# Kernel tuning notes

Hardware: AMD Instinct MI355X
Metric: run time of the kernel (lower is better)

## Reference

```python
import jax, jax.numpy as jnp
import numpy as np

N = 50000      # nodes
E = 800000     # edges (before self loops)
IN = 128       # in_ch
HID = 128      # hid (conv1 concat output)
OUT = 128      # out_ch
H = 4          # heads in conv1
NEG_SLOPE = 0.2


def setup_inputs() -> dict:
    key = jax.random.key(0)
    ks = jax.random.split(key, 16)
    s = 0.05
    return {
        "x": jax.random.normal(ks[0], (N, IN), dtype=jnp.float32),
        "edge_index": jax.random.randint(ks[1], (2, E), 0, N, dtype=jnp.int64),
        # conv1 params (heads=4, per-head dim HID//H)
        "W1l": jax.random.normal(ks[2], (IN, HID), dtype=jnp.float32) * s,
        "b1l": jnp.zeros((HID,), jnp.float32),
        "W1r": jax.random.normal(ks[3], (IN, HID), dtype=jnp.float32) * s,
        "b1r": jnp.zeros((HID,), jnp.float32),
        "att1": jax.random.normal(ks[4], (H, HID // H), dtype=jnp.float32) * s,
        "bias1": jnp.zeros((HID,), jnp.float32),
        # conv2 params (heads=1)
        "W2l": jax.random.normal(ks[5], (HID, OUT), dtype=jnp.float32) * s,
        "b2l": jnp.zeros((OUT,), jnp.float32),
        "W2r": jax.random.normal(ks[6], (HID, OUT), dtype=jnp.float32) * s,
        "b2r": jnp.zeros((OUT,), jnp.float32),
        "att2": jax.random.normal(ks[7], (1, OUT), dtype=jnp.float32) * s,
        "bias2": jnp.zeros((OUT,), jnp.float32),
    }


def gatv2_conv(x, src, dst, Wl, bl, Wr, br, att, heads):
    """PyG GATv2Conv (share_weights=False, concat=True).
    message(j->i): e = LeakyReLU(x_l[j] + x_r[i]); logit = <e, att>;
    softmax over edges per destination i; out_i = sum alpha * x_l[j].
    """
    n = x.shape[0]
    c = Wl.shape[1] // heads
    xl = (x @ Wl + bl).reshape(n, heads, c)   # source transform
    xr = (x @ Wr + br).reshape(n, heads, c)   # destination transform
    e = jax.nn.leaky_relu(xl[src] + xr[dst], NEG_SLOPE)      # [E, H, C]
    logits = jnp.einsum("ehc,hc->eh", e, att)                 # [E, H]
    m = jax.lax.stop_gradient(
        jax.ops.segment_max(logits, dst, num_segments=n))     # [N, H]
    p = jnp.exp(logits - m[dst])                              # [E, H]
    denom = jax.ops.segment_sum(p, dst, num_segments=n)       # [N, H]
    alpha = p / denom[dst]                                    # [E, H]
    out = jax.ops.segment_sum(xl[src] * alpha[..., None], dst,
                              num_segments=n)                 # [N, H, C]
    return out.reshape(n, heads * c)


def reference(x, edge_index, W1l, b1l, W1r, b1r, att1, bias1,
              W2l, b2l, W2r, b2r, att2, bias2):
    n = x.shape[0]
    # PyG default add_self_loops=True
    loops = jnp.arange(n, dtype=edge_index.dtype)
    src = jnp.concatenate([edge_index[0], loops])
    dst = jnp.concatenate([edge_index[1], loops])
    h = gatv2_conv(x, src, dst, W1l, b1l, W1r, b1r, att1, H) + bias1
    h = jax.nn.relu(h)
    out = gatv2_conv(h, src, dst, W2l, b2l, W2r, b2r, att2, 1) + bias2
    return out
```

## Files before the change

kernel.cpp:

```cpp
#include <hip/hip_runtime.h>
#include <hip/hip_bf16.h>

#define NODES 50000
#define NEDGE 800000
#define CH 128
#define NEG_SLOPE 0.2f
#define SCAN_CHUNK 2048
#define NBLK ((NODES + SCAN_CHUNK - 1) / SCAN_CHUNK)
#define NINF -1.0e30f
#define LOG2E 1.44269504088896340736f
#define RESCALE_THR 8.0f
#define NSLICE 400
#define SSLICE (NEDGE / NSLICE)
#define ZB ((NODES + 255) / 256)

typedef short short8 __attribute__((ext_vector_type(8)));
typedef float f32x4 __attribute__((ext_vector_type(4)));
typedef float f32x2 __attribute__((ext_vector_type(2)));

__device__ __forceinline__ unsigned fbits(float f) {
    union { float f; unsigned u; } v; v.f = f; return v.u;
}
__device__ __forceinline__ float asf(unsigned u) {
    union { float f; unsigned u; } v; v.u = u; return v.f;
}
__device__ __forceinline__ unsigned short f2bf(float f) {
    unsigned u = fbits(f);
    unsigned r = u + 0x7fff + ((u >> 16) & 1);
    return (unsigned short)(r >> 16);
}
__device__ __forceinline__ float bf2f(unsigned short h) {
    return asf(((unsigned)h) << 16);
}
__device__ __forceinline__ void bf8cvt2(uint4 u, f32x2* f) {
    f[0] = (f32x2){asf(u.x << 16), asf(u.x & 0xFFFF0000u)};
    f[1] = (f32x2){asf(u.y << 16), asf(u.y & 0xFFFF0000u)};
    f[2] = (f32x2){asf(u.z << 16), asf(u.z & 0xFFFF0000u)};
    f[3] = (f32x2){asf(u.w << 16), asf(u.w & 0xFFFF0000u)};
}
__device__ __forceinline__ int dset(int dst) {
    return (int)(((unsigned)dst * 8u) / 50000u);
}

__global__ __launch_bounds__(256) void prep_kernel(const void* idx, int* flag,
                                                   int* cnt,
                                                   const float* __restrict__ W0,
                                                   const float* __restrict__ W1,
                                                   const float* __restrict__ W2,
                                                   const float* __restrict__ W3,
                                                   unsigned short* __restrict__ wbase) {
    int b = (int)blockIdx.x;
    if (b < ZB) {
        int t = b * 256 + (int)threadIdx.x;
        if (t < NODES) cnt[t] = 0;
        if (b == 0 && threadIdx.x < 64) {
            const int* w = (const int*)idx;
            int nz = (w[2 * threadIdx.x + 1] != 0) ? 1 : 0;
            unsigned long long bal = __ballot(nz);
            if (threadIdx.x == 0) *flag = (bal == 0ull) ? 1 : 0;
        }
        return;
    }
    int wb = b - ZB;
    int which = wb >> 6;
    const float* W = (which == 0) ? W0 : (which == 1) ? W1 : (which == 2) ? W2 : W3;
    unsigned short* hiT = wbase + (size_t)which * 32768;
    unsigned short* loT = hiT + 16384;
    int i = (wb & 63) * 256 + (int)threadIdx.x;
    int k = i >> 7, n = i & 127;
    float f = W[i];
    unsigned short h = f2bf(f);
    unsigned short l = f2bf(f - bf2f(h));
    hiT[n * CH + k] = h;
    loT[n * CH + k] = l;
}

__global__ __launch_bounds__(256) void hist_part_kernel(const void* idx,
                                                        const int* flag,
                                                        int* cnt) {
    int set = blockIdx.x & 7;
    int slice = blockIdx.x >> 3;
    int base = slice * SSLICE;
    int endE = base + SSLICE;
    int i64 = *flag;
    const int* w = (const int*)idx;
    for (int e = base + (int)threadIdx.x; e < endE; e += 256) {
        int dst = i64 ? w[2 * (NEDGE + e)] : w[NEDGE + e];
        if (dset(dst) == set) atomicAdd(&cnt[dst], 1);
    }
}

__global__ __launch_bounds__(256) void scan1_kernel(const int* __restrict__ cnt,
                                                    int* __restrict__ bsum) {
    int base = blockIdx.x * SCAN_CHUNK + (int)threadIdx.x * 8;
    int s = 0;
    #pragma unroll
    for (int k = 0; k < 8; ++k) {
        int i = base + k;
        s += (i < NODES) ? cnt[i] : 0;
    }
    #pragma unroll
    for (int m = 1; m < 64; m <<= 1) s += __shfl_xor(s, m);
    __shared__ int ws[4];
    if ((threadIdx.x & 63) == 0) ws[threadIdx.x >> 6] = s;
    __syncthreads();
    if (threadIdx.x == 0) bsum[blockIdx.x] = ws[0] + ws[1] + ws[2] + ws[3];
}

__global__ __launch_bounds__(256) void scan3_kernel(const int* __restrict__ cnt,
                                                    const int* __restrict__ bsum,
                                                    int* __restrict__ offs,
                                                    int* __restrict__ cursor) {
    int tid = (int)threadIdx.x;
    int bpre = 0;
    #pragma unroll
    for (int b = 0; b < NBLK; ++b) bpre += (b < (int)blockIdx.x) ? bsum[b] : 0;

    int base = blockIdx.x * SCAN_CHUNK + tid * 8;
    int v[8];
    int s = 0;
    #pragma unroll
    for (int k = 0; k < 8; ++k) {
        int i = base + k;
        v[k] = (i < NODES) ? cnt[i] : 0;
        s += v[k];
    }
    int lane = tid & 63;
    int incl = s;
    #pragma unroll
    for (int m = 1; m < 64; m <<= 1) {
        int t = __shfl_up(incl, m);
        if (lane >= m) incl += t;
    }
    __shared__ int wtot[4];
    if (lane == 63) wtot[tid >> 6] = incl;
    __syncthreads();
    int w = tid >> 6;
    int wbase = 0;
    #pragma unroll
    for (int k = 0; k < 4; ++k) wbase += (k < w) ? wtot[k] : 0;
    int excl = bpre + wbase + (incl - s);
    #pragma unroll
    for (int k = 0; k < 8; ++k) {
        int i = base + k;
        if (i < NODES) { offs[i] = excl; cursor[i] = excl; }
        excl += v[k];
    }
    if (blockIdx.x == 0 && tid == 0) offs[NODES] = NEDGE;
}

__global__ __launch_bounds__(256) void scatter_part_kernel(const void* idx,
                                                           const int* flag,
                                                           int* cursor,
                                                           int* __restrict__ srcs) {
    int set = blockIdx.x & 7;
    int slice = blockIdx.x >> 3;
    int base = slice * SSLICE;
    int endE = base + SSLICE;
    int i64 = *flag;
    const int* w = (const int*)idx;
    for (int e = base + (int)threadIdx.x; e < endE; e += 256) {
        int dst = i64 ? w[2 * (NEDGE + e)] : w[NEDGE + e];
        if (dset(dst) == set) {
            int src = i64 ? w[2 * e] : w[e];
            int pos = atomicAdd(&cursor[dst], 1);
            srcs[pos] = src;
        }
    }
}

#define GR 64
#define LDP 136

__global__ __launch_bounds__(512) void gemm_dual_mfma(
        const float* __restrict__ X,
        const unsigned short* __restrict__ whTl, const unsigned short* __restrict__ wlTl,
        const unsigned short* __restrict__ whTr, const unsigned short* __restrict__ wlTr,
        const float* __restrict__ bl, const float* __restrict__ br,
        unsigned short* __restrict__ Ylb, float* __restrict__ Yr, int nrows) {
    __shared__ unsigned short xh[GR][LDP];
    __shared__ unsigned short xlo[GR][LDP];

    int r0 = blockIdx.x * GR;
    int tid = (int)threadIdx.x;

    {
        int row = tid >> 3;
        int c0 = (tid & 7) * 16;
        const float* src = X + (size_t)(r0 + row) * CH + c0;
        bool valid = (r0 + row) < nrows;
        #pragma unroll
        for (int j = 0; j < 16; j += 4) {
            float4 v = valid ? *(const float4*)(src + j)
                             : make_float4(0.f, 0.f, 0.f, 0.f);
            unsigned ux = fbits(v.x), uy = fbits(v.y);
            unsigned uz = fbits(v.z), uw = fbits(v.w);
            unsigned hx = ux & 0xFFFF0000u, hy = uy & 0xFFFF0000u;
            unsigned hz = uz & 0xFFFF0000u, hw = uw & 0xFFFF0000u;
            uint2 hp;
            hp.x = (ux >> 16) | hy;
            hp.y = (uz >> 16) | hw;
            float lx = v.x - asf(hx), ly = v.y - asf(hy);
            float lz = v.z - asf(hz), lw = v.w - asf(hw);
            uint2 lp;
            lp.x = (fbits(lx) >> 16) | (fbits(ly) & 0xFFFF0000u);
            lp.y = (fbits(lz) >> 16) | (fbits(lw) & 0xFFFF0000u);
            *(uint2*)&xh[row][c0 + j]  = hp;
            *(uint2*)&xlo[row][c0 + j] = lp;
        }
    }
    __syncthreads();

    int wave = tid >> 6;
    int lane = tid & 63;
    int l15 = lane & 15, q = lane >> 4;

    f32x4 acc[4][2];
    #pragma unroll
    for (int mt = 0; mt < 4; ++mt)
        #pragma unroll
        for (int nt = 0; nt < 2; ++nt) acc[mt][nt] = (f32x4)0.f;

    const unsigned short* bhp[2];
    const unsigned short* blp_[2];
    int ncol[2];
    #pragma unroll
    for (int nt = 0; nt < 2; ++nt) {
        int n = (wave * 2 + nt) * 16 + l15;
        ncol[nt] = n;
        int nn = n & 127;
        bhp[nt]  = ((n < CH) ? whTl : whTr) + (size_t)nn * CH;
        blp_[nt] = ((n < CH) ? wlTl : wlTr) + (size_t)nn * CH;
    }

    for (int kt = 0; kt < 4; ++kt) {
        int kofs = kt * 32 + q * 8;
        short8 ah[4], al[4];
        #pragma unroll
        for (int mt = 0; mt < 4; ++mt) {
            ah[mt] = *(const short8*)&xh[mt * 16 + l15][kofs];
            al[mt] = *(const short8*)&xlo[mt * 16 + l15][kofs];
        }
        #pragma unroll
        for (int nt = 0; nt < 2; ++nt) {
            short8 bh8 = *(const short8*)(bhp[nt] + kofs);
            short8 bl8 = *(const short8*)(blp_[nt] + kofs);
            #pragma unroll
            for (int mt = 0; mt < 4; ++mt) {
                acc[mt][nt] = __builtin_amdgcn_mfma_f32_16x16x32_bf16(
                                  ah[mt], bh8, acc[mt][nt], 0, 0, 0);
                acc[mt][nt] = __builtin_amdgcn_mfma_f32_16x16x32_bf16(
                                  al[mt], bh8, acc[mt][nt], 0, 0, 0);
                acc[mt][nt] = __builtin_amdgcn_mfma_f32_16x16x32_bf16(
                                  ah[mt], bl8, acc[mt][nt], 0, 0, 0);
            }
        }
    }

    #pragma unroll
    for (int nt = 0; nt < 2; ++nt) {
        int n = ncol[nt];
        int nc = n & 127;
        if (n < CH) {
            float bv = bl[nc];
            #pragma unroll
            for (int mt = 0; mt < 4; ++mt)
                #pragma unroll
                for (int reg = 0; reg < 4; ++reg) {
                    int row = r0 + mt * 16 + q * 4 + reg;
                    if (row < nrows)
                        Ylb[(size_t)row * CH + nc] = f2bf(acc[mt][nt][reg] + bv);
                }
        } else {
            float bv = br[nc];
            #pragma unroll
            for (int mt = 0; mt < 4; ++mt)
                #pragma unroll
                for (int reg = 0; reg < 4; ++reg) {
                    int row = r0 + mt * 16 + q * 4 + reg;
                    if (row < nrows)
                        Yr[(size_t)row * CH + nc] = acc[mt][nt][reg] + bv;
                }
        }
    }
}

__global__ __launch_bounds__(512) void gemm_dual_mfma_pl(
        const unsigned short* __restrict__ Ah, const unsigned short* __restrict__ Al,
        const unsigned short* __restrict__ whTl, const unsigned short* __restrict__ wlTl,
        const unsigned short* __restrict__ whTr, const unsigned short* __restrict__ wlTr,
        const float* __restrict__ bl, const float* __restrict__ br,
        unsigned short* __restrict__ Ylb, float* __restrict__ Yr, int nrows) {
    __shared__ unsigned short xh[GR][LDP];
    __shared__ unsigned short xlo[GR][LDP];

    int r0 = blockIdx.x * GR;
    int tid = (int)threadIdx.x;

    {
        int row = tid >> 3;
        int c0 = (tid & 7) * 16;
        int gr = r0 + row;
        if (gr > nrows - 1) gr = nrows - 1;
        const uint4* ph = (const uint4*)(Ah + (size_t)gr * CH + c0);
        const uint4* pl = (const uint4*)(Al + (size_t)gr * CH + c0);
        uint4 h0 = ph[0], h1 = ph[1];
        uint4 l0 = pl[0], l1 = pl[1];
        *(uint4*)&xh[row][c0]      = h0;
        *(uint4*)&xh[row][c0 + 8]  = h1;
        *(uint4*)&xlo[row][c0]     = l0;
        *(uint4*)&xlo[row][c0 + 8] = l1;
    }
    __syncthreads();

    int wave = tid >> 6;
    int lane = tid & 63;
    int l15 = lane & 15, q = lane >> 4;

    f32x4 acc[4][2];
    #pragma unroll
    for (int mt = 0; mt < 4; ++mt)
        #pragma unroll
        for (int nt = 0; nt < 2; ++nt) acc[mt][nt] = (f32x4)0.f;

    const unsigned short* bhp[2];
    const unsigned short* blp_[2];
    int ncol[2];
    #pragma unroll
    for (int nt = 0; nt < 2; ++nt) {
        int n = (wave * 2 + nt) * 16 + l15;
        ncol[nt] = n;
        int nn = n & 127;
        bhp[nt]  = ((n < CH) ? whTl : whTr) + (size_t)nn * CH;
        blp_[nt] = ((n < CH) ? wlTl : wlTr) + (size_t)nn * CH;
    }

    for (int kt = 0; kt < 4; ++kt) {
        int kofs = kt * 32 + q * 8;
        short8 ah[4], al[4];
        #pragma unroll
        for (int mt = 0; mt < 4; ++mt) {
            ah[mt] = *(const short8*)&xh[mt * 16 + l15][kofs];
            al[mt] = *(const short8*)&xlo[mt * 16 + l15][kofs];
        }
        #pragma unroll
        for (int nt = 0; nt < 2; ++nt) {
            short8 bh8 = *(const short8*)(bhp[nt] + kofs);
            short8 bl8 = *(const short8*)(blp_[nt] + kofs);
            #pragma unroll
            for (int mt = 0; mt < 4; ++mt) {
                acc[mt][nt] = __builtin_amdgcn_mfma_f32_16x16x32_bf16(
                                  ah[mt], bh8, acc[mt][nt], 0, 0, 0);
                acc[mt][nt] = __builtin_amdgcn_mfma_f32_16x16x32_bf16(
                                  al[mt], bh8, acc[mt][nt], 0, 0, 0);
                acc[mt][nt] = __builtin_amdgcn_mfma_f32_16x16x32_bf16(
                                  ah[mt], bl8, acc[mt][nt], 0, 0, 0);
            }
        }
    }

    #pragma unroll
    for (int nt = 0; nt < 2; ++nt) {
        int n = ncol[nt];
        int nc = n & 127;
        if (n < CH) {
            float bv = bl[nc];
            #pragma unroll
            for (int mt = 0; mt < 4; ++mt)
                #pragma unroll
                for (int reg = 0; reg < 4; ++reg) {
                    int row = r0 + mt * 16 + q * 4 + reg;
                    if (row < nrows)
                        Ylb[(size_t)row * CH + nc] = f2bf(acc[mt][nt][reg] + bv);
                }
        } else {
            float bv = br[nc];
            #pragma unroll
            for (int mt = 0; mt < 4; ++mt)
                #pragma unroll
                for (int reg = 0; reg < 4; ++reg) {
                    int row = r0 + mt * 16 + q * 4 + reg;
                    if (row < nrows)
                        Yr[(size_t)row * CH + nc] = acc[mt][nt][reg] + bv;
                }
        }
    }
}

template <int HEADS, bool RELU, bool SPLITOUT>
__global__ __launch_bounds__(256) void node_pass(
        const unsigned short* __restrict__ xlb,
        const float* __restrict__ xr,
        const float* __restrict__ att,
        const float* __restrict__ bias,
        const int* __restrict__ offs, const int* __restrict__ srcs,
        float* __restrict__ outf,
        unsigned short* __restrict__ outh, unsigned short* __restrict__ outl) {
    constexpr int GL = (CH / HEADS) / 8;
    int wave = (int)threadIdx.x >> 6;
    int i = blockIdx.x * 4 + wave;
    int lane = (int)threadIdx.x & 63;
    int g = lane >> 4;
    int l16 = lane & 15;
    int c0 = l16 * 8;

    f32x2 r2[4], a2[4], s2[4];
    {
        const float4* xrp = (const float4*)(xr + (size_t)i * CH + c0);
        float4 r0 = xrp[0], r1 = xrp[1];
        r2[0] = (f32x2){r0.x, r0.y}; r2[1] = (f32x2){r0.z, r0.w};
        r2[2] = (f32x2){r1.x, r1.y}; r2[3] = (f32x2){r1.z, r1.w};
        const float4* atp = (const float4*)(att + c0);
        float4 a0 = atp[0], a1 = atp[1];
        a2[0] = (f32x2){a0.x, a0.y} * LOG2E; a2[1] = (f32x2){a0.z, a0.w} * LOG2E;
        a2[2] = (f32x2){a1.x, a1.y} * LOG2E; a2[3] = (f32x2){a1.z, a1.w} * LOG2E;
    }
    uint4 us = *(const uint4*)(xlb + (size_t)i * CH + c0);
    bf8cvt2(us, s2);

    f32x2 td = (f32x2)0.f;
    #pragma unroll
    for (int k = 0; k < 4; ++k) {
        f32x2 z = s2[k] + r2[k];
        f32x2 l = __builtin_elementwise_max(z, z * NEG_SLOPE);
        td += l * a2[k];
    }
    float ts = td.x + td.y;
    #pragma unroll
    for (int msk = 1; msk < GL; msk <<= 1) ts += __shfl_xor(ts, msk);

    float m = ts;
    float d = (g == 0) ? 1.f : 0.f;
    f32x2 acc2[4];
    #pragma unroll
    for (int k = 0; k < 4; ++k) acc2[k] = (g == 0) ? s2[k] : (f32x2)0.f;

    int beg = offs[i], end = offs[i + 1];
    int deg = end - beg;
    int iters = (deg + 3) >> 2;
    if (iters > 0) {
        int last = end - 1;
        int e = beg + g;
        int si = srcs[min(e, last)];
        uint4 u = *(const uint4*)(xlb + (size_t)si * CH + c0);

        for (int it = 0; it < iters; ++it, e += 4) {
            bool valid = e < end;
            int sn = srcs[min(e + 4, last)];
            uint4 un = *(const uint4*)(xlb + (size_t)sn * CH + c0);

            f32x2 f2[4];
            bf8cvt2(u, f2);
            f32x2 td2 = (f32x2)0.f;
            #pragma unroll
            for (int k = 0; k < 4; ++k) {
                f32x2 z = f2[k] + r2[k];
                f32x2 l = __builtin_elementwise_max(z, z * NEG_SLOPE);
                td2 += l * a2[k];
            }
            float t = td2.x + td2.y;
            #pragma unroll
            for (int msk = 1; msk < GL; msk <<= 1) t += __shfl_xor(t, msk);
            t = valid ? t : NINF;

            if (__any(t > m + RESCALE_THR)) {
                float nm = fmaxf(m, t);
                float sc = exp2f(m - nm);
                float p  = exp2f(t - nm);
                d = d * sc + p;
                #pragma unroll
                for (int k = 0; k < 4; ++k) acc2[k] = acc2[k] * sc + f2[k] * p;
                m = nm;
            } else {
                float p = exp2f(t - m);
                d += p;
                #pragma unroll
                for (int k = 0; k < 4; ++k) acc2[k] += f2[k] * p;
            }
            u = un;
        }
    }

    #pragma unroll
    for (int msk = 16; msk <= 32; msk <<= 1) {
        float mo  = __shfl_xor(m, msk);
        float dof = __shfl_xor(d, msk);
        float nm = fmaxf(m, mo);
        float s0 = exp2f(m - nm), s1 = exp2f(mo - nm);
        d = d * s0 + dof * s1;
        #pragma unroll
        for (int k = 0; k < 4; ++k) {
            f32x2 ao;
            ao.x = __shfl_xor(acc2[k].x, msk);
            ao.y = __shfl_xor(acc2[k].y, msk);
            acc2[k] = acc2[k] * s0 + ao * s1;
        }
        m = nm;
    }

    if (g == 0) {
        float inv = 1.0f / d;
        const float4* bp = (const float4*)(bias + c0);
        float4 b0 = bp[0], b1 = bp[1];
        float bb[8] = {b0.x, b0.y, b0.z, b0.w, b1.x, b1.y, b1.z, b1.w};
        float o[8];
        #pragma unroll
        for (int k = 0; k < 4; ++k) {
            o[2*k]   = acc2[k].x * inv + bb[2*k];
            o[2*k+1] = acc2[k].y * inv + bb[2*k+1];
        }
        #pragma unroll
        for (int c = 0; c < 8; ++c)
            if (RELU) o[c] = fmaxf(o[c], 0.f);
        if (SPLITOUT) {
            unsigned hu[8];
            float lo[8];
            #pragma unroll
            for (int c = 0; c < 8; ++c) {
                hu[c] = fbits(o[c]) & 0xFFFF0000u;
                lo[c] = o[c] - asf(hu[c]);
            }
            uint4 ph, pl;
            ph.x = (hu[0] >> 16) | hu[1];  ph.y = (hu[2] >> 16) | hu[3];
            ph.z = (hu[4] >> 16) | hu[5];  ph.w = (hu[6] >> 16) | hu[7];
            pl.x = (fbits(lo[0]) >> 16) | (fbits(lo[1]) & 0xFFFF0000u);
            pl.y = (fbits(lo[2]) >> 16) | (fbits(lo[3]) & 0xFFFF0000u);
            pl.z = (fbits(lo[4]) >> 16) | (fbits(lo[5]) & 0xFFFF0000u);
            pl.w = (fbits(lo[6]) >> 16) | (fbits(lo[7]) & 0xFFFF0000u);
            *(uint4*)(outh + (size_t)i * CH + c0) = ph;
            *(uint4*)(outl + (size_t)i * CH + c0) = pl;
        } else {
            float4 w0 = make_float4(o[0], o[1], o[2], o[3]);
            float4 w1 = make_float4(o[4], o[5], o[6], o[7]);
            float4* op = (float4*)(outf + (size_t)i * CH + c0);
            op[0] = w0; op[1] = w1;
        }
    }
}

extern "C" void kernel_launch(void* const* d_in, const int* in_sizes, int n_in,
                              void* d_out, int out_size, void* d_ws, size_t ws_size,
                              hipStream_t stream) {
    const float* x     = (const float*)d_in[0];
    const void*  eidx  = d_in[1];
    const float* W1l   = (const float*)d_in[2];
    const float* b1l   = (const float*)d_in[3];
    const float* W1r   = (const float*)d_in[4];
    const float* b1r   = (const float*)d_in[5];
    const float* att1  = (const float*)d_in[6];
    const float* bias1 = (const float*)d_in[7];
    const float* W2l   = (const float*)d_in[8];
    const float* b2l   = (const float*)d_in[9];
    const float* W2r   = (const float*)d_in[10];
    const float* b2r   = (const float*)d_in[11];
    const float* att2  = (const float*)d_in[12];
    const float* bias2 = (const float*)d_in[13];
    float* out = (float*)d_out;

    unsigned short* xlb = (unsigned short*)d_ws;
    float* xr = (float*)(xlb + (size_t)NODES * CH);
    unsigned short* hbh = (unsigned short*)(xr + (size_t)NODES * CH);
    unsigned short* hbl = hbh + (size_t)NODES * CH;
    int* offs   = (int*)(hbl + (size_t)NODES * CH);
    int* cnt    = offs + (NODES + 1);
    int* cursor = cnt + NODES;
    int* srcs   = cursor + NODES;
    int* flag   = srcs + NEDGE;
    int* bsum   = flag + 1;
    unsigned short* wbuf =
        (unsigned short*)(((uintptr_t)(bsum + NBLK) + 15) & ~(uintptr_t)15);
    unsigned short* w1lh = wbuf;              unsigned short* w1ll = wbuf + 16384;
    unsigned short* w1rh = wbuf + 32768;      unsigned short* w1rl = wbuf + 49152;
    unsigned short* w2lh = wbuf + 65536;      unsigned short* w2ll = wbuf + 81920;
    unsigned short* w2rh = wbuf + 98304;      unsigned short* w2rl = wbuf + 114688;

    const int GG = (NODES + GR - 1) / GR;
    const int PG = NSLICE * 8;

    prep_kernel<<<ZB + 256, 256, 0, stream>>>(eidx, flag, cnt,
                                              W1l, W1r, W2l, W2r, wbuf);
    hist_part_kernel<<<PG, 256, 0, stream>>>(eidx, flag, cnt);
    scan1_kernel<<<NBLK, 256, 0, stream>>>(cnt, bsum);
    scan3_kernel<<<NBLK, 256, 0, stream>>>(cnt, bsum, offs, cursor);
    scatter_part_kernel<<<PG, 256, 0, stream>>>(eidx, flag, cursor, srcs);

    gemm_dual_mfma<<<GG, 512, 0, stream>>>(x, w1lh, w1ll, w1rh, w1rl,
                                           b1l, b1r, xlb, xr, NODES);
    node_pass<4, true, true><<<(NODES + 3) / 4, 256, 0, stream>>>(
        xlb, xr, att1, bias1, offs, srcs, nullptr, hbh, hbl);

    gemm_dual_mfma_pl<<<GG, 512, 0, stream>>>(hbh, hbl, w2lh, w2ll, w2rh, w2rl,
                                              b2l, b2r, xlb, xr, NODES);
    node_pass<1, false, false><<<(NODES + 3) / 4, 256, 0, stream>>>(
        xlb, xr, att2, bias2, offs, srcs, out, nullptr, nullptr);
}
```

Before: 335.8 us.

## Fuse degree histogram into layer-1 GEMM launch and merge scan kernels

```diff
diff --git a/kernel.cpp b/kernel.cpp
--- a/kernel.cpp
+++ b/kernel.cpp
@@ -12,7 +12,11 @@
 #define RESCALE_THR 8.0f
 #define NSLICE 400
 #define SSLICE (NEDGE / NSLICE)
+#define HSLICE 4000
+#define NHS (NEDGE / HSLICE)
 #define ZB ((NODES + 255) / 256)
+#define GR 64
+#define GGC ((NODES + GR - 1) / GR)
 
 typedef short short8 __attribute__((ext_vector_type(8)));
 typedef float f32x4 __attribute__((ext_vector_type(4)));
@@ -75,46 +79,22 @@
     loT[n * CH + k] = l;
 }
 
-__global__ __launch_bounds__(256) void hist_part_kernel(const void* idx,
-                                                        const int* flag,
-                                                        int* cnt) {
-    int set = blockIdx.x & 7;
-    int slice = blockIdx.x >> 3;
-    int base = slice * SSLICE;
-    int endE = base + SSLICE;
-    int i64 = *flag;
-    const int* w = (const int*)idx;
-    for (int e = base + (int)threadIdx.x; e < endE; e += 256) {
-        int dst = i64 ? w[2 * (NEDGE + e)] : w[NEDGE + e];
-        if (dset(dst) == set) atomicAdd(&cnt[dst], 1);
-    }
-}
-
-__global__ __launch_bounds__(256) void scan1_kernel(const int* __restrict__ cnt,
-                                                    int* __restrict__ bsum) {
-    int base = blockIdx.x * SCAN_CHUNK + (int)threadIdx.x * 8;
-    int s = 0;
-    #pragma unroll
-    for (int k = 0; k < 8; ++k) {
-        int i = base + k;
-        s += (i < NODES) ? cnt[i] : 0;
-    }
-    #pragma unroll
-    for (int m = 1; m < 64; m <<= 1) s += __shfl_xor(s, m);
-    __shared__ int ws[4];
-    if ((threadIdx.x & 63) == 0) ws[threadIdx.x >> 6] = s;
+#define LDP 136
+
+__global__ __launch_bounds__(256) void scan3m_kernel(const int* __restrict__ cnt,
+                                                     int* __restrict__ offs,
+                                                     int* __restrict__ cursor) {
+    int tid = (int)threadIdx.x;
+
+    int lim = (int)blockIdx.x * SCAN_CHUNK;
+    int pre = 0;
+    for (int idx = tid; idx < lim; idx += 256) pre += cnt[idx];
+    #pragma unroll
+    for (int m = 1; m < 64; m <<= 1) pre += __shfl_xor(pre, m);
+    __shared__ int pw[4];
+    if ((tid & 63) == 0) pw[tid >> 6] = pre;
     __syncthreads();
-    if (threadIdx.x == 0) bsum[blockIdx.x] = ws[0] + ws[1] + ws[2] + ws[3];
-}
-
-__global__ __launch_bounds__(256) void scan3_kernel(const int* __restrict__ cnt,
-                                                    const int* __restrict__ bsum,
-                                                    int* __restrict__ offs,
-                                                    int* __restrict__ cursor) {
-    int tid = (int)threadIdx.x;
-    int bpre = 0;
-    #pragma unroll
-    for (int b = 0; b < NBLK; ++b) bpre += (b < (int)blockIdx.x) ? bsum[b] : 0;
+    int bpre = pw[0] + pw[1] + pw[2] + pw[3];
 
     int base = blockIdx.x * SCAN_CHUNK + tid * 8;
     int v[8];
@@ -169,17 +149,30 @@
     }
 }
 
-#define GR 64
-#define LDP 136
-
-__global__ __launch_bounds__(512) void gemm_dual_mfma(
+__global__ __launch_bounds__(512) void gemm1_hist(
         const float* __restrict__ X,
         const unsigned short* __restrict__ whTl, const unsigned short* __restrict__ wlTl,
         const unsigned short* __restrict__ whTr, const unsigned short* __restrict__ wlTr,
         const float* __restrict__ bl, const float* __restrict__ br,
-        unsigned short* __restrict__ Ylb, float* __restrict__ Yr, int nrows) {
+        unsigned short* __restrict__ Ylb, float* __restrict__ Yr, int nrows,
+        const void* idx, const int* flag, int* cnt) {
     __shared__ unsigned short xh[GR][LDP];
     __shared__ unsigned short xlo[GR][LDP];
+
+    if (blockIdx.x >= GGC) {
+        int gb = (int)blockIdx.x;
+        int set = gb & 7;
+        int slice = (gb - GGC) >> 3;
+        int base = slice * HSLICE;
+        int endE = base + HSLICE;
+        int i64 = *flag;
+        const int* w = (const int*)idx;
+        for (int e = base + (int)threadIdx.x; e < endE; e += 512) {
+            int dst = i64 ? w[2 * (NEDGE + e)] : w[NEDGE + e];
+            if (dset(dst) == set) atomicAdd(&cnt[dst], 1);
+        }
+        return;
+    }
 
     int r0 = blockIdx.x * GR;
     int tid = (int)threadIdx.x;
@@ -574,23 +567,24 @@
     unsigned short* w2lh = wbuf + 65536;      unsigned short* w2ll = wbuf + 81920;
     unsigned short* w2rh = wbuf + 98304;      unsigned short* w2rl = wbuf + 114688;
 
-    const int GG = (NODES + GR - 1) / GR;
     const int PG = NSLICE * 8;
+    const int FG = GGC + NHS * 8;
 
     prep_kernel<<<ZB + 256, 256, 0, stream>>>(eidx, flag, cnt,
                                               W1l, W1r, W2l, W2r, wbuf);
-    hist_part_kernel<<<PG, 256, 0, stream>>>(eidx, flag, cnt);
-    scan1_kernel<<<NBLK, 256, 0, stream>>>(cnt, bsum);
-    scan3_kernel<<<NBLK, 256, 0, stream>>>(cnt, bsum, offs, cursor);
+
+    gemm1_hist<<<FG, 512, 0, stream>>>(x, w1lh, w1ll, w1rh, w1rl,
+                                       b1l, b1r, xlb, xr, NODES,
+                                       eidx, flag, cnt);
+
+    scan3m_kernel<<<NBLK, 256, 0, stream>>>(cnt, offs, cursor);
     scatter_part_kernel<<<PG, 256, 0, stream>>>(eidx, flag, cursor, srcs);
 
-    gemm_dual_mfma<<<GG, 512, 0, stream>>>(x, w1lh, w1ll, w1rh, w1rl,
-                                           b1l, b1r, xlb, xr, NODES);
     node_pass<4, true, true><<<(NODES + 3) / 4, 256, 0, stream>>>(
         xlb, xr, att1, bias1, offs, srcs, nullptr, hbh, hbl);
 
-    gemm_dual_mfma_pl<<<GG, 512, 0, stream>>>(hbh, hbl, w2lh, w2ll, w2rh, w2rl,
-                                              b2l, b2r, xlb, xr, NODES);
+    gemm_dual_mfma_pl<<<GGC, 512, 0, stream>>>(hbh, hbl, w2lh, w2ll, w2rh, w2rl,
+                                               b2l, b2r, xlb, xr, NODES);
     node_pass<1, false, false><<<(NODES + 3) / 4, 256, 0, stream>>>(
         xlb, xr, att2, bias2, offs, srcs, out, nullptr, nullptr);
 }
```

Result: no change. 342.2 us (+1.9%).
